# Kernel optimization log

Measured on AMD Instinct MI355X. Metric: run time of the kernel, lower is better.

The kernel has to match this reference:

```python
import jax, jax.numpy as jnp
import numpy as np
from jax import lax

NS, C_IN, C_FEAT, CROP = 16, 3, 32, 256


def _conv(x, w, b):
    # 3x3 stride-1 'SAME' conv == padding=1 in torch
    y = lax.conv_general_dilated(x, w, (1, 1), 'SAME',
                                 dimension_numbers=('NCHW', 'OIHW', 'NCHW'))
    return y + b[None, :, None, None]


def _lrn(x, size=5, alpha=1e-4, beta=0.75, k=1.0):
    # PyTorch LocalResponseNorm: x / (k + alpha/size * sum_window x^2)^beta
    pad = size // 2
    sq = jnp.pad(x * x, ((0, 0), (pad, pad), (0, 0), (0, 0)))
    c = x.shape[1]
    win = sum(sq[:, i:i + c] for i in range(size))
    return x / (k + (alpha / size) * win) ** beta


def setup_inputs() -> dict:
    key = jax.random.key(0)
    ks = jax.random.split(key, 6)
    s = 0.05
    h = np.hanning(CROP).astype(np.float32)
    cos_window = jnp.asarray(np.outer(h, h))
    return {
        'z': jax.random.normal(ks[0], (NS, C_IN, CROP, CROP), jnp.float32),
        'w1': jax.random.normal(ks[1], (C_FEAT, C_IN, 3, 3), jnp.float32) * s,
        'b1': jax.random.normal(ks[2], (C_FEAT,), jnp.float32) * s,
        'w2': jax.random.normal(ks[3], (C_FEAT, C_FEAT, 3, 3), jnp.float32) * s,
        'b2': jax.random.normal(ks[4], (C_FEAT,), jnp.float32) * s,
        'cos_window': cos_window,
        'wf': jax.random.normal(ks[5], (1, C_FEAT, CROP, CROP // 2 + 1, 2), jnp.float32) * s,
    }


def reference(z, w1, b1, w2, b2, cos_window, wf):
    # feature extractor: conv -> relu -> conv -> LRN
    f = jax.nn.relu(_conv(z, w1, b1))
    f = _lrn(_conv(f, w2, b2))
    f = f * cos_window  # (ns, 32, crop, crop)
    zf = jnp.fft.rfft2(f, axes=(-2, -1))  # (ns, 32, crop, crop//2+1) complex
    # faithful to source: w_star = conj(wf), and the loop always uses w_star[0, 1]
    # (fixed channel 1) multiplied with zf[c, l], accumulated over l. wf is detached.
    wc = lax.stop_gradient(wf[0, 1, :, :, 0] - 1j * wf[0, 1, :, :, 1])
    ftrans = wc[None, None] * jnp.sum(zf, axis=1, keepdims=True)  # (ns,1,crop,crop//2+1)
    response = jnp.fft.irfft2(ftrans, s=(CROP, CROP), axes=(-2, -1))
    return response  # (ns, 1, crop, crop)
```

## Files before the change

### kernel.cpp

```cpp
#include <hip/hip_runtime.h>
#include <math.h>

#define NS   16
#define CIN  3
#define CF   32
#define CROP 256
#define KH   129

typedef _Float16 half8  __attribute__((ext_vector_type(8)));
typedef _Float16 half4v __attribute__((ext_vector_type(4)));
typedef _Float16 half2v __attribute__((ext_vector_type(2)));
typedef float    f32x4  __attribute__((ext_vector_type(4)));
typedef unsigned int u32x4 __attribute__((ext_vector_type(4)));

__device__ __forceinline__ half8 neg8(half8 v) {
    u32x4 u = __builtin_bit_cast(u32x4, v);
    u ^= (u32x4){0x80008000u, 0x80008000u, 0x80008000u, 0x80008000u};
    return __builtin_bit_cast(half8, u);
}

__device__ __forceinline__ int swz8(int b, int nb) {
    int q = nb >> 3, r = nb & 7;
    int x = b & 7, o = b >> 3;
    return (x < r ? x * (q + 1) : r * (q + 1) + (x - r) * q) + o;
}

#define X_OFF 0
#define Z_OFF 21504
#define LDS_BYTES 23904

__device__ __forceinline__ int xaddr(int q, int s) {
    return X_OFF + (q << 6) + ((s ^ ((q >> 1) & 3)) << 4);
}

__device__ __forceinline__ int pi_of(int co) {
    int h = co >> 3, j = co & 7;
    return (j < 4) ? (h * 4 + j) : (16 + h * 4 + j - 4);
}
__device__ __forceinline__ int cinv_of(int p) {
    int h = (p & 15) >> 2;
    int j = (p & 3) + ((p >= 16) ? 4 : 0);
    return h * 8 + j;
}

__device__ __forceinline__ void split_pair(float v0, float v1,
                                           half2v* hp, half2v* lp) {
    _Float16 h0 = (_Float16)v0, h1 = (_Float16)v1;
    *hp = (half2v){h0, h1};
    *lp = (half2v){(_Float16)(v0 - (float)h0), (_Float16)(v1 - (float)h1)};
}

__global__ __launch_bounds__(256)
void prep(const float* __restrict__ w1, const float* __restrict__ w2,
          _Float16* __restrict__ w1pk, _Float16* __restrict__ w2lin,
          _Float16* __restrict__ TAh, _Float16* __restrict__ TAl,
          _Float16* __restrict__ G1h, _Float16* __restrict__ G1l,
          _Float16* __restrict__ G3h, _Float16* __restrict__ G3l,
          _Float16* __restrict__ TCh, _Float16* __restrict__ TCl)
{
    const int bid = blockIdx.x, tid = threadIdx.x;

    if (bid >= 134) {
        int base = (bid - 134) * 4096;
        #pragma unroll
        for (int i = 0; i < 16; ++i) {
            int e = base + tid + i * 256;
            if (e < 9216) {
                int co = e / 288;
                int r  = e - co * 288;
                int ci = r / 9, k9 = r - ci * 9;
                w2lin[(k9 * 32 + pi_of(co)) * 32 + ci] = (_Float16)w2[e];
            } else if (e < 9344) {
                int t = e - 9216;
                int lane = t & 63;
                int p = (t >> 6) * 16 + (lane & 15);
                int c = cinv_of(p);
                #pragma unroll
                for (int j = 0; j < 8; ++j) {
                    int k = ((lane >> 4) << 3) + j;
                    w1pk[t * 8 + j] = (k < 27) ? (_Float16)w1[c * 27 + k]
                                               : (_Float16)0.f;
                }
            }
        }
        return;
    }

    __shared__ float cs[256], sn[256];
    {
        float s, c;
        sincosf(0.02454369260617025967f * (float)tid, &s, &c);
        cs[tid] = c; sn[tid] = s;
    }
    __syncthreads();

    if (bid < 34) {
        int base = bid * 1024 + tid;
        #pragma unroll
        for (int i = 0; i < 4; ++i) {
            int p = base + i * 256;
            int j0 = (p & 3) * 2, lane = (p >> 2) & 63, q = p >> 8;
            int nt = q % 17, ks = q / 17;
            int x0 = ks * 32 + ((lane >> 4) << 3) + j0;
            int c = nt * 16 + (lane & 15);
            float v0 = 0.f, v1 = 0.f;
            if (c <= 128) {
                v0 =  cs[(x0 * c) & 255];
                v1 =  cs[((x0 + 1) * c) & 255];
            } else if (c >= 136 && c <= 264) {
                int cc = c - 136;
                v0 = -sn[(x0 * cc) & 255];
                v1 = -sn[((x0 + 1) * cc) & 255];
            }
            half2v hv, lv; split_pair(v0, v1, &hv, &lv);
            ((half2v*)TAh)[p] = hv; ((half2v*)TAl)[p] = lv;
        }
    } else if (bid < 98) {
        int base = (bid - 34) * 1024 + tid;
        #pragma unroll
        for (int i = 0; i < 4; ++i) {
            int p = base + i * 256;
            int j0 = (p & 3) * 2, lane = (p >> 2) & 63, q = p >> 8;
            int nt = q & 15, ks = q >> 4;
            int kk0 = ks * 32 + ((lane >> 4) << 3) + j0;
            int m  = nt * 16 + (lane & 15);
            int part = kk0 >> 8;
            int y0 = kk0 & 255;
            int i0 = (y0 * m) & 255, i1 = ((y0 + 1) * m) & 255;
            float cv0 = cs[i0], s0 = sn[i0], cv1 = cs[i1], s1 = sn[i1];
            half2v hv, lv;
            float a0 = part ? s0 : cv0,  a1 = part ? s1 : cv1;
            split_pair(a0, a1, &hv, &lv);
            ((half2v*)G1h)[p] = hv; ((half2v*)G1l)[p] = lv;
            a0 = (part ? -s0 : cv0) * (1.f/256.f);
            a1 = (part ? -s1 : cv1) * (1.f/256.f);
            split_pair(a0, a1, &hv, &lv);
            ((half2v*)G3h)[p] = hv; ((half2v*)G3l)[p] = lv;
        }
    } else {
        int base = (bid - 98) * 1024 + tid;
        #pragma unroll
        for (int i = 0; i < 4; ++i) {
            int p = base + i * 256;
            int j0 = (p & 3) * 2, lane = (p >> 2) & 63, q = p >> 8;
            int nt = q & 15, ks = q >> 4;
            int kk0 = ks * 32 + ((lane >> 4) << 3) + j0;
            int x  = nt * 16 + (lane & 15);
            int part = (kk0 >= 144) ? 1 : 0;
            int k0 = kk0 - part * 144;
            float v0 = 0.f, v1 = 0.f;
            if (k0 <= 128) {
                float w0 = (k0 == 0 || k0 == 128) ? 1.f : 2.f;
                int ii = (k0 * x) & 255;
                v0 = (part ? -w0 * sn[ii] : w0 * cs[ii]) * (1.f/256.f);
            }
            int k1 = k0 + 1;
            if (k1 <= 128) {
                float w1w = (k1 == 0 || k1 == 128) ? 1.f : 2.f;
                int ii = (k1 * x) & 255;
                v1 = (part ? -w1w * sn[ii] : w1w * cs[ii]) * (1.f/256.f);
            }
            half2v hv, lv; split_pair(v0, v1, &hv, &lv);
            ((half2v*)TCh)[p] = hv; ((half2v*)TCl)[p] = lv;
        }
    }
}

__global__ __launch_bounds__(256, 5)
void fused_features(const float* __restrict__ z,
                    const _Float16* __restrict__ w1pk,
                    const float* __restrict__ b1,
                    const _Float16* __restrict__ w2lin,
                    const float* __restrict__ b2,
                    const float* __restrict__ cosw,
                    _Float16* __restrict__ g2h, _Float16* __restrict__ g2l)
{
    __shared__ __align__(16) unsigned char smem[LDS_BYTES];
    _Float16* ztile = (_Float16*)(smem + Z_OFF);

    const int tid  = threadIdx.x;
    const int lane = tid & 63;
    const int wv   = tid >> 6;
    const int l15  = lane & 15;
    const int lhi  = lane >> 4;

    const int n  = blockIdx.z;
    const int bx = blockIdx.x, by = blockIdx.y;
    const int fy0 = by * 16 - 1;
    const int fx0 = bx * 16 - 1;

    const int zy0 = by * 16 - 2;
    const int zx0 = bx * 16 - 2;
    for (int idx = tid; idx < CIN * 400; idx += 256) {
        int ci = idx / 400;
        int r  = idx - ci * 400;
        int yy = r / 20, xx = r - yy * 20;
        int gy = zy0 + yy, gx = zx0 + xx;
        float v = 0.0f;
        if ((unsigned)gy < CROP && (unsigned)gx < CROP)
            v = z[((n * CIN + ci) * CROP + gy) * CROP + gx];
        ztile[idx] = (_Float16)v;
    }

    half8 w1f0 = *(const half8*)(w1pk + lane * 8);
    half8 w1f1 = *(const half8*)(w1pk + 512 + lane * 8);
    float bias1v[2][4], bias2v[2][4];
    #pragma unroll
    for (int cg = 0; cg < 2; ++cg)
        #pragma unroll
        for (int r = 0; r < 4; ++r) {
            bias1v[cg][r] = b1[8 * lhi + 4 * cg + r];
            bias2v[cg][r] = b2[8 * lhi + 4 * cg + r];
        }

    int offs[8];
    #pragma unroll
    for (int j = 0; j < 8; ++j) {
        int k = lhi * 8 + j;
        int ci = k / 9, rr = k - ci * 9;
        int ky = rr / 3, kx = rr - ky * 3;
        offs[j] = (k < 27) ? (ci * 400 + ky * 20 + kx) : 0;
    }
    __syncthreads();

    const f32x4 zero4 = {0.f, 0.f, 0.f, 0.f};
    for (int t = wv; t < 21; t += 4) {
        int qp = t * 16 + l15;
        int qpc = qp < 324 ? qp : 323;
        int y = qpc / 18, x = qpc - y * 18;
        const _Float16* zb = ztile + y * 20 + x;
        half8 bfrag;
        #pragma unroll
        for (int j = 0; j < 8; ++j) bfrag[j] = zb[offs[j]];
        f32x4 d0 = __builtin_amdgcn_mfma_f32_16x16x32_f16(w1f0, bfrag, zero4, 0, 0, 0);
        f32x4 d1 = __builtin_amdgcn_mfma_f32_16x16x32_f16(w1f1, bfrag, zero4, 0, 0, 0);
        int gy = fy0 + y, gx = fx0 + x;
        bool ok = ((unsigned)gy < CROP) && ((unsigned)gx < CROP) && (qp < 324);
        half8 o8;
        #pragma unroll
        for (int r = 0; r < 4; ++r) {
            float v0 = ok ? fmaxf(d0[r] + bias1v[0][r], 0.f) : 0.f;
            float v1 = ok ? fmaxf(d1[r] + bias1v[1][r], 0.f) : 0.f;
            o8[r]     = (_Float16)v0;
            o8[4 + r] = (_Float16)v1;
        }
        *(half8*)(smem + xaddr(qp, lhi)) = o8;
    }
    __syncthreads();

    f32x4 acc[4][2];
    #pragma unroll
    for (int tt = 0; tt < 4; ++tt)
        #pragma unroll
        for (int cg = 0; cg < 2; ++cg)
            #pragma unroll
            for (int r = 0; r < 4; ++r)
                acc[tt][cg][r] = bias2v[cg][r];

    #pragma unroll
    for (int k9 = 0; k9 < 9; ++k9) {
        const int ky = k9 / 3, kx = k9 - 3 * ky;
        half8 af0 = *(const half8*)(w2lin + (k9 * 32 + l15)      * 32 + lhi * 8);
        half8 af1 = *(const half8*)(w2lin + (k9 * 32 + l15 + 16) * 32 + lhi * 8);
        #pragma unroll
        for (int tt = 0; tt < 4; ++tt) {
            int q = (wv * 4 + tt + ky) * 18 + l15 + kx;
            half8 bf = *(const half8*)(smem + xaddr(q, lhi));
            acc[tt][0] = __builtin_amdgcn_mfma_f32_16x16x32_f16(af0, bf, acc[tt][0], 0, 0, 0);
            acc[tt][1] = __builtin_amdgcn_mfma_f32_16x16x32_f16(af1, bf, acc[tt][1], 0, 0, 0);
        }
    }

    const bool bot = (lhi == 0), top = (lhi == 3);
    #pragma unroll
    for (int tt = 0; tt < 4; ++tt) {
        float aA0 = acc[tt][0][0], aA1 = acc[tt][0][1],
              aA2 = acc[tt][0][2], aA3 = acc[tt][0][3];
        float aB0 = acc[tt][1][0], aB1 = acc[tt][1][1],
              aB2 = acc[tt][1][2], aB3 = acc[tt][1][3];
        float sA0 = aA0 * aA0, sA1 = aA1 * aA1, sA2 = aA2 * aA2, sA3 = aA3 * aA3;
        float sB0 = aB0 * aB0, sB1 = aB1 * aB1, sB2 = aB2 * aB2, sB3 = aB3 * aB3;
        int up = (lane + 16) & 63, dn = (lane + 48) & 63;
        float em2 = __shfl(sB2, dn); em2 = bot ? 0.f : em2;
        float em1 = __shfl(sB3, dn); em1 = bot ? 0.f : em1;
        float ep8 = __shfl(sA0, up); ep8 = top ? 0.f : ep8;
        float ep9 = __shfl(sA1, up); ep9 = top ? 0.f : ep9;
        float s = 0.f, win = em2 + em1 + sA0 + sA1 + sA2;
        float t2, f;
        t2 = 2e-5f * win; f = fmaf(t2, fmaf(t2, 0.65625f, -0.75f), 1.0f);
        s = fmaf(aA0, f, s);  win += sA3 - em2;
        t2 = 2e-5f * win; f = fmaf(t2, fmaf(t2, 0.65625f, -0.75f), 1.0f);
        s = fmaf(aA1, f, s);  win += sB0 - em1;
        t2 = 2e-5f * win; f = fmaf(t2, fmaf(t2, 0.65625f, -0.75f), 1.0f);
        s = fmaf(aA2, f, s);  win += sB1 - sA0;
        t2 = 2e-5f * win; f = fmaf(t2, fmaf(t2, 0.65625f, -0.75f), 1.0f);
        s = fmaf(aA3, f, s);  win += sB2 - sA1;
        t2 = 2e-5f * win; f = fmaf(t2, fmaf(t2, 0.65625f, -0.75f), 1.0f);
        s = fmaf(aB0, f, s);  win += sB3 - sA2;
        t2 = 2e-5f * win; f = fmaf(t2, fmaf(t2, 0.65625f, -0.75f), 1.0f);
        s = fmaf(aB1, f, s);  win += ep8 - sA3;
        t2 = 2e-5f * win; f = fmaf(t2, fmaf(t2, 0.65625f, -0.75f), 1.0f);
        s = fmaf(aB2, f, s);  win += ep9 - sB0;
        t2 = 2e-5f * win; f = fmaf(t2, fmaf(t2, 0.65625f, -0.75f), 1.0f);
        s = fmaf(aB3, f, s);
        s += __shfl_xor(s, 16);
        s += __shfl_xor(s, 32);
        if (lhi == 0) {
            int gy = by * 16 + wv * 4 + tt, gx = bx * 16 + l15;
            float val = s * cosw[gy * CROP + gx];
            _Float16 h = (_Float16)val;
            int o = (n * CROP + gy) * CROP + gx;
            g2h[o] = h;
            g2l[o] = (_Float16)(val - (float)h);
        }
    }
}

__global__ __launch_bounds__(256, 4)
void fft_rows(const _Float16* __restrict__ g2h, const _Float16* __restrict__ g2l,
              const _Float16* __restrict__ TAh, const _Float16* __restrict__ TAl,
              _Float16* __restrict__ Zth, _Float16* __restrict__ Ztl)
{
    __shared__ f32x4 part[2][3][64];
    const int lane = threadIdx.x & 63;
    const int w = threadIdx.x >> 6;
    const int u = w >> 1, kh = w & 1;
    const int bsw = swz8(blockIdx.x, 2176);
    const int unit = bsw * 2 + u;
    const int mt = unit / 17, nt = unit - mt * 17;
    const int l15 = lane & 15, lhi = lane >> 4;
    const int rowA = mt * 16 + l15;

    f32x4 a0 = {}, a1 = {}, a2 = {};
    #pragma unroll
    for (int i = 0; i < 4; ++i) {
        const int ks = kh * 4 + i;
        const int ao = rowA * 256 + ks * 32 + lhi * 8;
        half8 Ah = *(const half8*)(g2h + ao);
        half8 Al = *(const half8*)(g2l + ao);
        const int bo = ((ks * 17 + nt) * 64 + lane) * 8;
        half8 Bh = *(const half8*)(TAh + bo);
        half8 Bl = *(const half8*)(TAl + bo);
        a0 = __builtin_amdgcn_mfma_f32_16x16x32_f16(Ah, Bh, a0, 0, 0, 0);
        a1 = __builtin_amdgcn_mfma_f32_16x16x32_f16(Ah, Bl, a1, 0, 0, 0);
        a2 = __builtin_amdgcn_mfma_f32_16x16x32_f16(Al, Bh, a2, 0, 0, 0);
    }
    if (kh) {
        part[u][0][lane] = a0; part[u][1][lane] = a1; part[u][2][lane] = a2;
    }
    __syncthreads();
    if (kh) return;
    a0 += part[u][0][lane]; a1 += part[u][1][lane]; a2 += part[u][2][lane];

    f32x4 acc;
    #pragma unroll
    for (int r = 0; r < 4; ++r) acc[r] = a0[r] + a1[r] + a2[r];

    const int rowD = mt * 16 + lhi * 4;
    const int n = rowD >> 8, y = rowD & 255;
    int c = nt * 16 + l15;
    int row_k = -1, koff = 0;
    if (c <= 128)                  { row_k = c;       koff = 0;   }
    else if (c >= 136 && c <= 264) { row_k = c - 136; koff = 256; }
    if (row_k >= 0) {
        half4v hv, lv;
        #pragma unroll
        for (int r = 0; r < 4; ++r) {
            float v = acc[r];
            _Float16 h = (_Float16)v;
            hv[r] = h; lv[r] = (_Float16)(v - (float)h);
        }
        size_t o = (size_t)(n * 129 + row_k) * 512 + koff + y;
        *(half4v*)(Zth + o) = hv;
        *(half4v*)(Ztl + o) = lv;
    }
}

__global__ __launch_bounds__(256, 4)
void fft_cols_mul(const _Float16* __restrict__ Zth, const _Float16* __restrict__ Ztl,
                  const _Float16* __restrict__ G1h, const _Float16* __restrict__ G1l,
                  const float* __restrict__ wf,
                  _Float16* __restrict__ Ph, _Float16* __restrict__ Pl)
{
    __shared__ f32x4 part[2][6][64];
    const int lane = threadIdx.x & 63;
    const int w = threadIdx.x >> 6;
    const int u = w >> 1, kh = w & 1;
    const int bsw = swz8(blockIdx.x, 1032);
    const int unit = bsw * 2 + u;
    const int mt = unit >> 4, nt = unit & 15;
    const int l15 = lane & 15, lhi = lane >> 4;
    const int rowA = mt * 16 + l15;

    f32x4 r0 = {}, r1 = {}, r2 = {}, i0 = {}, i1 = {}, i2 = {};
    #pragma unroll
    for (int i = 0; i < 4; ++i) {
        const int ks = kh * 4 + i;
        const int ao0 = rowA * 512 + ks * 32 + lhi * 8;
        half8 Ah0 = *(const half8*)(Zth + ao0);
        half8 Al0 = *(const half8*)(Ztl + ao0);
        half8 Ah1 = *(const half8*)(Zth + ao0 + 256);
        half8 Al1 = *(const half8*)(Ztl + ao0 + 256);
        const int bo0 = ((ks * 16 + nt) * 64 + lane) * 8;
        half8 B0h = *(const half8*)(G1h + bo0);
        half8 B0l = *(const half8*)(G1l + bo0);
        half8 B1h_ = *(const half8*)(G1h + bo0 + 65536);
        half8 B1l_ = *(const half8*)(G1l + bo0 + 65536);
        half8 nB1h = neg8(B1h_), nB1l = neg8(B1l_);
        r0 = __builtin_amdgcn_mfma_f32_16x16x32_f16(Ah0, B0h,  r0, 0, 0, 0);
        r1 = __builtin_amdgcn_mfma_f32_16x16x32_f16(Ah0, B0l,  r1, 0, 0, 0);
        r2 = __builtin_amdgcn_mfma_f32_16x16x32_f16(Al0, B0h,  r2, 0, 0, 0);
        r0 = __builtin_amdgcn_mfma_f32_16x16x32_f16(Ah1, B1h_, r0, 0, 0, 0);
        r1 = __builtin_amdgcn_mfma_f32_16x16x32_f16(Ah1, B1l_, r1, 0, 0, 0);
        r2 = __builtin_amdgcn_mfma_f32_16x16x32_f16(Al1, B1h_, r2, 0, 0, 0);
        i0 = __builtin_amdgcn_mfma_f32_16x16x32_f16(Ah0, nB1h, i0, 0, 0, 0);
        i1 = __builtin_amdgcn_mfma_f32_16x16x32_f16(Ah0, nB1l, i1, 0, 0, 0);
        i2 = __builtin_amdgcn_mfma_f32_16x16x32_f16(Al0, nB1h, i2, 0, 0, 0);
        i0 = __builtin_amdgcn_mfma_f32_16x16x32_f16(Ah1, B0h,  i0, 0, 0, 0);
        i1 = __builtin_amdgcn_mfma_f32_16x16x32_f16(Ah1, B0l,  i1, 0, 0, 0);
        i2 = __builtin_amdgcn_mfma_f32_16x16x32_f16(Al1, B0h,  i2, 0, 0, 0);
    }
    if (kh) {
        part[u][0][lane] = r0; part[u][1][lane] = r1; part[u][2][lane] = r2;
        part[u][3][lane] = i0; part[u][4][lane] = i1; part[u][5][lane] = i2;
    }
    __syncthreads();
    if (kh) return;
    r0 += part[u][0][lane]; r1 += part[u][1][lane]; r2 += part[u][2][lane];
    i0 += part[u][3][lane]; i1 += part[u][4][lane]; i2 += part[u][5][lane];

    const int rowP0 = mt * 16 + lhi * 4;
    const int m = nt * 16 + l15;
    const float* wf1 = wf + 256 * 129 * 2;
    int n_ = rowP0 / 129;
    int k_ = rowP0 - n_ * 129;
    #pragma unroll
    for (int r = 0; r < 4; ++r) {
        float wr = wf1[(m * 129 + k_) * 2 + 0];
        float wi = wf1[(m * 129 + k_) * 2 + 1];
        float fr = r0[r] + r1[r] + r2[r];
        float fi = i0[r] + i1[r] + i2[r];
        float pr = wr * fr + wi * fi;
        float pi = wr * fi - wi * fr;
        size_t o = (size_t)(rowP0 + r) * 512 + m;
        _Float16 h;
        h = (_Float16)pr; Ph[o] = h;       Pl[o] = (_Float16)(pr - (float)h);
        h = (_Float16)pi; Ph[o + 256] = h; Pl[o + 256] = (_Float16)(pi - (float)h);
        if (++k_ == 129) { k_ = 0; ++n_; }
    }
}

__global__ __launch_bounds__(256, 4)
void fft_cols_inv(const _Float16* __restrict__ Ph, const _Float16* __restrict__ Pl,
                  const _Float16* __restrict__ G3h, const _Float16* __restrict__ G3l,
                  _Float16* __restrict__ Bth, _Float16* __restrict__ Btl)
{
    __shared__ f32x4 part[2][6][64];
    const int lane = threadIdx.x & 63;
    const int w = threadIdx.x >> 6;
    const int u = w >> 1, kh = w & 1;
    const int bsw = swz8(blockIdx.x, 1032);
    const int unit = bsw * 2 + u;
    const int mt = unit >> 4, nt = unit & 15;
    const int l15 = lane & 15, lhi = lane >> 4;
    const int rowA = mt * 16 + l15;

    f32x4 r0 = {}, r1 = {}, r2 = {}, i0 = {}, i1 = {}, i2 = {};
    #pragma unroll
    for (int i = 0; i < 4; ++i) {
        const int ks = kh * 4 + i;
        const int ao0 = rowA * 512 + ks * 32 + lhi * 8;
        half8 Ah0 = *(const half8*)(Ph + ao0);
        half8 Al0 = *(const half8*)(Pl + ao0);
        half8 Ah1 = *(const half8*)(Ph + ao0 + 256);
        half8 Al1 = *(const half8*)(Pl + ao0 + 256);
        const int bo0 = ((ks * 16 + nt) * 64 + lane) * 8;
        half8 B0h = *(const half8*)(G3h + bo0);
        half8 B0l = *(const half8*)(G3l + bo0);
        half8 B1h_ = *(const half8*)(G3h + bo0 + 65536);
        half8 B1l_ = *(const half8*)(G3l + bo0 + 65536);
        half8 nB1h = neg8(B1h_), nB1l = neg8(B1l_);
        r0 = __builtin_amdgcn_mfma_f32_16x16x32_f16(Ah0, B0h,  r0, 0, 0, 0);
        r1 = __builtin_amdgcn_mfma_f32_16x16x32_f16(Ah0, B0l,  r1, 0, 0, 0);
        r2 = __builtin_amdgcn_mfma_f32_16x16x32_f16(Al0, B0h,  r2, 0, 0, 0);
        r0 = __builtin_amdgcn_mfma_f32_16x16x32_f16(Ah1, B1h_, r0, 0, 0, 0);
        r1 = __builtin_amdgcn_mfma_f32_16x16x32_f16(Ah1, B1l_, r1, 0, 0, 0);
        r2 = __builtin_amdgcn_mfma_f32_16x16x32_f16(Al1, B1h_, r2, 0, 0, 0);
        i0 = __builtin_amdgcn_mfma_f32_16x16x32_f16(Ah0, nB1h, i0, 0, 0, 0);
        i1 = __builtin_amdgcn_mfma_f32_16x16x32_f16(Ah0, nB1l, i1, 0, 0, 0);
        i2 = __builtin_amdgcn_mfma_f32_16x16x32_f16(Al0, nB1h, i2, 0, 0, 0);
        i0 = __builtin_amdgcn_mfma_f32_16x16x32_f16(Ah1, B0h,  i0, 0, 0, 0);
        i1 = __builtin_amdgcn_mfma_f32_16x16x32_f16(Ah1, B0l,  i1, 0, 0, 0);
        i2 = __builtin_amdgcn_mfma_f32_16x16x32_f16(Al1, B0h,  i2, 0, 0, 0);
    }
    if (kh) {
        part[u][0][lane] = r0; part[u][1][lane] = r1; part[u][2][lane] = r2;
        part[u][3][lane] = i0; part[u][4][lane] = i1; part[u][5][lane] = i2;
    }
    __syncthreads();
    if (kh) return;
    r0 += part[u][0][lane]; r1 += part[u][1][lane]; r2 += part[u][2][lane];
    i0 += part[u][3][lane]; i1 += part[u][4][lane]; i2 += part[u][5][lane];

    const int rowP0 = mt * 16 + lhi * 4;
    const int y = nt * 16 + l15;
    int n_ = rowP0 / 129;
    int k_ = rowP0 - n_ * 129;
    #pragma unroll
    for (int r = 0; r < 4; ++r) {
        size_t base = (size_t)(n_ * 256 + y) * 288 + k_;
        float v = r0[r] + r1[r] + r2[r];
        _Float16 h = (_Float16)v;
        Bth[base] = h;  Btl[base] = (_Float16)(v - (float)h);
        float v2 = i0[r] + i1[r] + i2[r];
        _Float16 h2 = (_Float16)v2;
        Bth[base + 144] = h2;  Btl[base + 144] = (_Float16)(v2 - (float)h2);
        if (++k_ == 129) { k_ = 0; ++n_; }
    }
}

__global__ __launch_bounds__(256, 4)
void irfft_rows(const _Float16* __restrict__ Bth, const _Float16* __restrict__ Btl,
                const _Float16* __restrict__ TCh, const _Float16* __restrict__ TCl,
                float* __restrict__ out)
{
    __shared__ f32x4 part[2][3][64];
    const int lane = threadIdx.x & 63;
    const int w = threadIdx.x >> 6;
    const int u = w >> 1, kh = w & 1;
    const int bsw = swz8(blockIdx.x, 2048);
    const int unit = bsw * 2 + u;
    const int mt = unit >> 4, nt = unit & 15;
    const int l15 = lane & 15, lhi = lane >> 4;
    const int rowA = mt * 16 + l15;

    f32x4 a0 = {}, a1 = {}, a2 = {};
    #pragma unroll
    for (int i = 0; i < 5; ++i) {
        if (kh && i == 4) break;
        const int ks = kh * 5 + i;
        const int ao = rowA * 288 + ks * 32 + lhi * 8;
        half8 Ah = *(const half8*)(Bth + ao);
        half8 Al = *(const half8*)(Btl + ao);
        const int bo = ((ks * 16 + nt) * 64 + lane) * 8;
        half8 Bh = *(const half8*)(TCh + bo);
        half8 Bl = *(const half8*)(TCl + bo);
        a0 = __builtin_amdgcn_mfma_f32_16x16x32_f16(Ah, Bh, a0, 0, 0, 0);
        a1 = __builtin_amdgcn_mfma_f32_16x16x32_f16(Ah, Bl, a1, 0, 0, 0);
        a2 = __builtin_amdgcn_mfma_f32_16x16x32_f16(Al, Bh, a2, 0, 0, 0);
    }
    if (kh) {
        part[u][0][lane] = a0; part[u][1][lane] = a1; part[u][2][lane] = a2;
    }
    __syncthreads();
    if (kh) return;
    a0 += part[u][0][lane]; a1 += part[u][1][lane]; a2 += part[u][2][lane];

    const int rowD = mt * 16 + lhi * 4;
    const int x = nt * 16 + l15;
    #pragma unroll
    for (int r = 0; r < 4; ++r)
        out[(size_t)(rowD + r) * 256 + x] = a0[r] + a1[r] + a2[r];
}

extern "C" void kernel_launch(void* const* d_in, const int* in_sizes, int n_in,
                              void* d_out, int out_size, void* d_ws, size_t ws_size,
                              hipStream_t stream)
{
    const float* z    = (const float*)d_in[0];
    const float* w1   = (const float*)d_in[1];
    const float* b1   = (const float*)d_in[2];
    const float* w2   = (const float*)d_in[3];
    const float* b2   = (const float*)d_in[4];
    const float* cosw = (const float*)d_in[5];
    const float* wf   = (const float*)d_in[6];
    float* out = (float*)d_out;

    char* p = (char*)d_ws;
    auto take = [&](size_t bytes) {
        char* r = p; p += (bytes + 255) & ~(size_t)255; return r;
    };
    _Float16* g2h = (_Float16*)take(4096 * 256 * 2);
    _Float16* g2l = (_Float16*)take(4096 * 256 * 2);
    _Float16* Zth = (_Float16*)take(2064 * 512 * 2);
    _Float16* Ztl = (_Float16*)take(2064 * 512 * 2);
    _Float16* Ph  = (_Float16*)take(2064 * 512 * 2);
    _Float16* Pl  = (_Float16*)take(2064 * 512 * 2);
    _Float16* Bth = (_Float16*)take(4096 * 288 * 2);
    _Float16* Btl = (_Float16*)take(4096 * 288 * 2);
    _Float16* TAh = (_Float16*)take(69632 * 2);
    _Float16* TAl = (_Float16*)take(69632 * 2);
    _Float16* G1h = (_Float16*)take(131072 * 2);
    _Float16* G1l = (_Float16*)take(131072 * 2);
    _Float16* G3h = (_Float16*)take(131072 * 2);
    _Float16* G3l = (_Float16*)take(131072 * 2);
    _Float16* TCh = (_Float16*)take(73728 * 2);
    _Float16* TCl = (_Float16*)take(73728 * 2);
    _Float16* w1pk  = (_Float16*)take(1024 * 2);
    _Float16* w2lin = (_Float16*)take(9216 * 2);

    prep<<<137, 256, 0, stream>>>(w1, w2, w1pk, w2lin, TAh, TAl,
                                  G1h, G1l, G3h, G3l, TCh, TCl);
    fused_features<<<dim3(16, 16, NS), 256, 0, stream>>>(z, w1pk, b1, w2lin, b2,
                                                         cosw, g2h, g2l);
    fft_rows<<<2176, 256, 0, stream>>>(g2h, g2l, TAh, TAl, Zth, Ztl);
    fft_cols_mul<<<1032, 256, 0, stream>>>(Zth, Ztl, G1h, G1l, wf, Ph, Pl);
    fft_cols_inv<<<1032, 256, 0, stream>>>(Ph, Pl, G3h, G3l, Bth, Btl);
    irfft_rows<<<2048, 256, 0, stream>>>(Bth, Btl, TCh, TCl, out);
}
```

Measured before the change: 103.9 us.

## Move twiddle table generation into fft_rows and split column FFT K across four waves

The G1/G3/TC twiddle-table generation moves out of the prep kernel into 100 extra blocks appended to fft_rows. This shortens prep, which sits ahead of fused_features on the critical path, and lets those tables be built alongside the row FFT. The column FFT kernels now give each block one output tile, with all four waves splitting the K dimension and reducing through LDS. That doubles the grid to 2064 blocks for more parallelism, at the cost of a larger LDS reduction and more blocks each doing less work.

Result: faster. 101.2 us (-2.5%).

```diff
diff --git a/kernel.cpp b/kernel.cpp
--- a/kernel.cpp
+++ b/kernel.cpp
@@ -53,15 +53,12 @@
 __global__ __launch_bounds__(256)
 void prep(const float* __restrict__ w1, const float* __restrict__ w2,
           _Float16* __restrict__ w1pk, _Float16* __restrict__ w2lin,
-          _Float16* __restrict__ TAh, _Float16* __restrict__ TAl,
-          _Float16* __restrict__ G1h, _Float16* __restrict__ G1l,
-          _Float16* __restrict__ G3h, _Float16* __restrict__ G3l,
-          _Float16* __restrict__ TCh, _Float16* __restrict__ TCl)
+          _Float16* __restrict__ TAh, _Float16* __restrict__ TAl)
 {
     const int bid = blockIdx.x, tid = threadIdx.x;
 
-    if (bid >= 134) {
-        int base = (bid - 134) * 4096;
+    if (bid >= 34) {
+        int base = (bid - 34) * 4096;
         #pragma unroll
         for (int i = 0; i < 16; ++i) {
             int e = base + tid + i * 256;
@@ -94,75 +91,25 @@
     }
     __syncthreads();
 
-    if (bid < 34) {
-        int base = bid * 1024 + tid;
-        #pragma unroll
-        for (int i = 0; i < 4; ++i) {
-            int p = base + i * 256;
-            int j0 = (p & 3) * 2, lane = (p >> 2) & 63, q = p >> 8;
-            int nt = q % 17, ks = q / 17;
-            int x0 = ks * 32 + ((lane >> 4) << 3) + j0;
-            int c = nt * 16 + (lane & 15);
-            float v0 = 0.f, v1 = 0.f;
-            if (c <= 128) {
-                v0 =  cs[(x0 * c) & 255];
-                v1 =  cs[((x0 + 1) * c) & 255];
-            } else if (c >= 136 && c <= 264) {
-                int cc = c - 136;
-                v0 = -sn[(x0 * cc) & 255];
-                v1 = -sn[((x0 + 1) * cc) & 255];
-            }
-            half2v hv, lv; split_pair(v0, v1, &hv, &lv);
-            ((half2v*)TAh)[p] = hv; ((half2v*)TAl)[p] = lv;
-        }
-    } else if (bid < 98) {
-        int base = (bid - 34) * 1024 + tid;
-        #pragma unroll
-        for (int i = 0; i < 4; ++i) {
-            int p = base + i * 256;
-            int j0 = (p & 3) * 2, lane = (p >> 2) & 63, q = p >> 8;
-            int nt = q & 15, ks = q >> 4;
-            int kk0 = ks * 32 + ((lane >> 4) << 3) + j0;
-            int m  = nt * 16 + (lane & 15);
-            int part = kk0 >> 8;
-            int y0 = kk0 & 255;
-            int i0 = (y0 * m) & 255, i1 = ((y0 + 1) * m) & 255;
-            float cv0 = cs[i0], s0 = sn[i0], cv1 = cs[i1], s1 = sn[i1];
-            half2v hv, lv;
-            float a0 = part ? s0 : cv0,  a1 = part ? s1 : cv1;
-            split_pair(a0, a1, &hv, &lv);
-            ((half2v*)G1h)[p] = hv; ((half2v*)G1l)[p] = lv;
-            a0 = (part ? -s0 : cv0) * (1.f/256.f);
-            a1 = (part ? -s1 : cv1) * (1.f/256.f);
-            split_pair(a0, a1, &hv, &lv);
-            ((half2v*)G3h)[p] = hv; ((half2v*)G3l)[p] = lv;
-        }
-    } else {
-        int base = (bid - 98) * 1024 + tid;
-        #pragma unroll
-        for (int i = 0; i < 4; ++i) {
-            int p = base + i * 256;
-            int j0 = (p & 3) * 2, lane = (p >> 2) & 63, q = p >> 8;
-            int nt = q & 15, ks = q >> 4;
-            int kk0 = ks * 32 + ((lane >> 4) << 3) + j0;
-            int x  = nt * 16 + (lane & 15);
-            int part = (kk0 >= 144) ? 1 : 0;
-            int k0 = kk0 - part * 144;
-            float v0 = 0.f, v1 = 0.f;
-            if (k0 <= 128) {
-                float w0 = (k0 == 0 || k0 == 128) ? 1.f : 2.f;
-                int ii = (k0 * x) & 255;
-                v0 = (part ? -w0 * sn[ii] : w0 * cs[ii]) * (1.f/256.f);
-            }
-            int k1 = k0 + 1;
-            if (k1 <= 128) {
-                float w1w = (k1 == 0 || k1 == 128) ? 1.f : 2.f;
-                int ii = (k1 * x) & 255;
-                v1 = (part ? -w1w * sn[ii] : w1w * cs[ii]) * (1.f/256.f);
-            }
-            half2v hv, lv; split_pair(v0, v1, &hv, &lv);
-            ((half2v*)TCh)[p] = hv; ((half2v*)TCl)[p] = lv;
-        }
+    int base = bid * 1024 + tid;
+    #pragma unroll
+    for (int i = 0; i < 4; ++i) {
+        int p = base + i * 256;
+        int j0 = (p & 3) * 2, lane = (p >> 2) & 63, q = p >> 8;
+        int nt = q % 17, ks = q / 17;
+        int x0 = ks * 32 + ((lane >> 4) << 3) + j0;
+        int c = nt * 16 + (lane & 15);
+        float v0 = 0.f, v1 = 0.f;
+        if (c <= 128) {
+            v0 =  cs[(x0 * c) & 255];
+            v1 =  cs[((x0 + 1) * c) & 255];
+        } else if (c >= 136 && c <= 264) {
+            int cc = c - 136;
+            v0 = -sn[(x0 * cc) & 255];
+            v1 = -sn[((x0 + 1) * cc) & 255];
+        }
+        half2v hv, lv; split_pair(v0, v1, &hv, &lv);
+        ((half2v*)TAh)[p] = hv; ((half2v*)TAl)[p] = lv;
     }
 }
 
@@ -319,11 +266,77 @@
 __global__ __launch_bounds__(256, 4)
 void fft_rows(const _Float16* __restrict__ g2h, const _Float16* __restrict__ g2l,
               const _Float16* __restrict__ TAh, const _Float16* __restrict__ TAl,
-              _Float16* __restrict__ Zth, _Float16* __restrict__ Ztl)
+              _Float16* __restrict__ Zth, _Float16* __restrict__ Ztl,
+              _Float16* __restrict__ G1h, _Float16* __restrict__ G1l,
+              _Float16* __restrict__ G3h, _Float16* __restrict__ G3l,
+              _Float16* __restrict__ TCh, _Float16* __restrict__ TCl)
 {
     __shared__ f32x4 part[2][3][64];
-    const int lane = threadIdx.x & 63;
-    const int w = threadIdx.x >> 6;
+    __shared__ float cs[256], sn[256];
+    const int tid = threadIdx.x;
+
+    if (blockIdx.x >= 2176) {
+        int tb = blockIdx.x - 2176;
+        {
+            float s, c;
+            sincosf(0.02454369260617025967f * (float)tid, &s, &c);
+            cs[tid] = c; sn[tid] = s;
+        }
+        __syncthreads();
+        if (tb < 64) {
+            int base = tb * 1024 + tid;
+            #pragma unroll
+            for (int i = 0; i < 4; ++i) {
+                int p = base + i * 256;
+                int j0 = (p & 3) * 2, lane = (p >> 2) & 63, q = p >> 8;
+                int nt = q & 15, ks = q >> 4;
+                int kk0 = ks * 32 + ((lane >> 4) << 3) + j0;
+                int m  = nt * 16 + (lane & 15);
+                int pt = kk0 >> 8;
+                int y0 = kk0 & 255;
+                int i0 = (y0 * m) & 255, i1 = ((y0 + 1) * m) & 255;
+                float cv0 = cs[i0], s0 = sn[i0], cv1 = cs[i1], s1 = sn[i1];
+                half2v hv, lv;
+                float a0 = pt ? s0 : cv0,  a1 = pt ? s1 : cv1;
+                split_pair(a0, a1, &hv, &lv);
+                ((half2v*)G1h)[p] = hv; ((half2v*)G1l)[p] = lv;
+                a0 = (pt ? -s0 : cv0) * (1.f/256.f);
+                a1 = (pt ? -s1 : cv1) * (1.f/256.f);
+                split_pair(a0, a1, &hv, &lv);
+                ((half2v*)G3h)[p] = hv; ((half2v*)G3l)[p] = lv;
+            }
+        } else {
+            int base = (tb - 64) * 1024 + tid;
+            #pragma unroll
+            for (int i = 0; i < 4; ++i) {
+                int p = base + i * 256;
+                int j0 = (p & 3) * 2, lane = (p >> 2) & 63, q = p >> 8;
+                int nt = q & 15, ks = q >> 4;
+                int kk0 = ks * 32 + ((lane >> 4) << 3) + j0;
+                int x  = nt * 16 + (lane & 15);
+                int pt = (kk0 >= 144) ? 1 : 0;
+                int k0 = kk0 - pt * 144;
+                float v0 = 0.f, v1 = 0.f;
+                if (k0 <= 128) {
+                    float w0 = (k0 == 0 || k0 == 128) ? 1.f : 2.f;
+                    int ii = (k0 * x) & 255;
+                    v0 = (pt ? -w0 * sn[ii] : w0 * cs[ii]) * (1.f/256.f);
+                }
+                int k1 = k0 + 1;
+                if (k1 <= 128) {
+                    float w1w = (k1 == 0 || k1 == 128) ? 1.f : 2.f;
+                    int ii = (k1 * x) & 255;
+                    v1 = (pt ? -w1w * sn[ii] : w1w * cs[ii]) * (1.f/256.f);
+                }
+                half2v hv, lv; split_pair(v0, v1, &hv, &lv);
+                ((half2v*)TCh)[p] = hv; ((half2v*)TCl)[p] = lv;
+            }
+        }
+        return;
+    }
+
+    const int lane = tid & 63;
+    const int w = tid >> 6;
     const int u = w >> 1, kh = w & 1;
     const int bsw = swz8(blockIdx.x, 2176);
     const int unit = bsw * 2 + u;
@@ -382,20 +395,18 @@
                   const float* __restrict__ wf,
                   _Float16* __restrict__ Ph, _Float16* __restrict__ Pl)
 {
-    __shared__ f32x4 part[2][6][64];
+    __shared__ f32x4 part[3][6][64];
     const int lane = threadIdx.x & 63;
-    const int w = threadIdx.x >> 6;
-    const int u = w >> 1, kh = w & 1;
-    const int bsw = swz8(blockIdx.x, 1032);
-    const int unit = bsw * 2 + u;
+    const int kh = threadIdx.x >> 6;
+    const int unit = swz8(blockIdx.x, 2064);
     const int mt = unit >> 4, nt = unit & 15;
     const int l15 = lane & 15, lhi = lane >> 4;
     const int rowA = mt * 16 + l15;
 
     f32x4 r0 = {}, r1 = {}, r2 = {}, i0 = {}, i1 = {}, i2 = {};
     #pragma unroll
-    for (int i = 0; i < 4; ++i) {
-        const int ks = kh * 4 + i;
+    for (int i = 0; i < 2; ++i) {
+        const int ks = kh * 2 + i;
         const int ao0 = rowA * 512 + ks * 32 + lhi * 8;
         half8 Ah0 = *(const half8*)(Zth + ao0);
         half8 Al0 = *(const half8*)(Ztl + ao0);
@@ -421,13 +432,17 @@
         i2 = __builtin_amdgcn_mfma_f32_16x16x32_f16(Al1, B0h,  i2, 0, 0, 0);
     }
     if (kh) {
-        part[u][0][lane] = r0; part[u][1][lane] = r1; part[u][2][lane] = r2;
-        part[u][3][lane] = i0; part[u][4][lane] = i1; part[u][5][lane] = i2;
+        part[kh - 1][0][lane] = r0; part[kh - 1][1][lane] = r1;
+        part[kh - 1][2][lane] = r2; part[kh - 1][3][lane] = i0;
+        part[kh - 1][4][lane] = i1; part[kh - 1][5][lane] = i2;
     }
     __syncthreads();
     if (kh) return;
-    r0 += part[u][0][lane]; r1 += part[u][1][lane]; r2 += part[u][2][lane];
-    i0 += part[u][3][lane]; i1 += part[u][4][lane]; i2 += part[u][5][lane];
+    #pragma unroll
+    for (int g = 0; g < 3; ++g) {
+        r0 += part[g][0][lane]; r1 += part[g][1][lane]; r2 += part[g][2][lane];
+        i0 += part[g][3][lane]; i1 += part[g][4][lane]; i2 += part[g][5][lane];
+    }
 
     const int rowP0 = mt * 16 + lhi * 4;
     const int m = nt * 16 + l15;
@@ -455,20 +470,18 @@
                   const _Float16* __restrict__ G3h, const _Float16* __restrict__ G3l,
                   _Float16* __restrict__ Bth, _Float16* __restrict__ Btl)
 {
-    __shared__ f32x4 part[2][6][64];
+    __shared__ f32x4 part[3][6][64];
     const int lane = threadIdx.x & 63;
-    const int w = threadIdx.x >> 6;
-    const int u = w >> 1, kh = w & 1;
-    const int bsw = swz8(blockIdx.x, 1032);
-    const int unit = bsw * 2 + u;
+    const int kh = threadIdx.x >> 6;
+    const int unit = swz8(blockIdx.x, 2064);
     const int mt = unit >> 4, nt = unit & 15;
     const int l15 = lane & 15, lhi = lane >> 4;
     const int rowA = mt * 16 + l15;
 
     f32x4 r0 = {}, r1 = {}, r2 = {}, i0 = {}, i1 = {}, i2 = {};
     #pragma unroll
-    for (int i = 0; i < 4; ++i) {
-        const int ks = kh * 4 + i;
+    for (int i = 0; i < 2; ++i) {
+        const int ks = kh * 2 + i;
         const int ao0 = rowA * 512 + ks * 32 + lhi * 8;
         half8 Ah0 = *(const half8*)(Ph + ao0);
         half8 Al0 = *(const half8*)(Pl + ao0);
@@ -494,13 +507,17 @@
         i2 = __builtin_amdgcn_mfma_f32_16x16x32_f16(Al1, B0h,  i2, 0, 0, 0);
     }
     if (kh) {
-        part[u][0][lane] = r0; part[u][1][lane] = r1; part[u][2][lane] = r2;
-        part[u][3][lane] = i0; part[u][4][lane] = i1; part[u][5][lane] = i2;
+        part[kh - 1][0][lane] = r0; part[kh - 1][1][lane] = r1;
+        part[kh - 1][2][lane] = r2; part[kh - 1][3][lane] = i0;
+        part[kh - 1][4][lane] = i1; part[kh - 1][5][lane] = i2;
     }
     __syncthreads();
     if (kh) return;
-    r0 += part[u][0][lane]; r1 += part[u][1][lane]; r2 += part[u][2][lane];
-    i0 += part[u][3][lane]; i1 += part[u][4][lane]; i2 += part[u][5][lane];
+    #pragma unroll
+    for (int g = 0; g < 3; ++g) {
+        r0 += part[g][0][lane]; r1 += part[g][1][lane]; r2 += part[g][2][lane];
+        i0 += part[g][3][lane]; i1 += part[g][4][lane]; i2 += part[g][5][lane];
+    }
 
     const int rowP0 = mt * 16 + lhi * 4;
     const int y = nt * 16 + l15;
@@ -599,12 +616,12 @@
     _Float16* w1pk  = (_Float16*)take(1024 * 2);
     _Float16* w2lin = (_Float16*)take(9216 * 2);
 
-    prep<<<137, 256, 0, stream>>>(w1, w2, w1pk, w2lin, TAh, TAl,
-                                  G1h, G1l, G3h, G3l, TCh, TCl);
+    prep<<<37, 256, 0, stream>>>(w1, w2, w1pk, w2lin, TAh, TAl);
     fused_features<<<dim3(16, 16, NS), 256, 0, stream>>>(z, w1pk, b1, w2lin, b2,
                                                          cosw, g2h, g2l);
-    fft_rows<<<2176, 256, 0, stream>>>(g2h, g2l, TAh, TAl, Zth, Ztl);
-    fft_cols_mul<<<1032, 256, 0, stream>>>(Zth, Ztl, G1h, G1l, wf, Ph, Pl);
-    fft_cols_inv<<<1032, 256, 0, stream>>>(Ph, Pl, G3h, G3l, Bth, Btl);
+    fft_rows<<<2276, 256, 0, stream>>>(g2h, g2l, TAh, TAl, Zth, Ztl,
+                                       G1h, G1l, G3h, G3l, TCh, TCl);
+    fft_cols_mul<<<2064, 256, 0, stream>>>(Zth, Ztl, G1h, G1l, wf, Ph, Pl);
+    fft_cols_inv<<<2064, 256, 0, stream>>>(Ph, Pl, G3h, G3l, Bth, Btl);
     irfft_rows<<<2048, 256, 0, stream>>>(Bth, Btl, TCh, TCl, out);
 }
```
